# Performance work log

Measured on AMD Instinct MI355X. Metric: run time of the kernel, lower is better.

Reference implementation:

```python
import jax, jax.numpy as jnp
import numpy as np

N_HEADS = 16


def setup_inputs() -> dict:
    key = jax.random.key(0)
    ks = jax.random.split(key, 5)
    B, S, D = 2, 2048, 1024
    scale = 1.0 / np.sqrt(D)
    return {
        "x": jax.random.normal(ks[0], (B, S, D), dtype=jnp.float32),
        "w_in": jax.random.normal(ks[1], (3 * D, D), dtype=jnp.float32) * scale,
        "b_in": jax.random.normal(ks[2], (3 * D,), dtype=jnp.float32) * 0.01,
        "w_out": jax.random.normal(ks[3], (D, D), dtype=jnp.float32) * scale,
        "b_out": jax.random.normal(ks[4], (D,), dtype=jnp.float32) * 0.01,
        "mask": 1,
    }


def reference(x, w_in, b_in, w_out, b_out, mask):
    b, s, d = x.shape
    h = N_HEADS
    dh = d // h
    # fused QKV projection (torch Linear: x @ W^T + b)
    qkv = jnp.einsum("bsd,ed->bse", x, w_in) + b_in  # [b, s, 3d]
    q, k, v = jnp.split(qkv, 3, axis=-1)
    # [b, s, d] -> [b, h, s, dh]
    q = q.reshape(b, s, h, dh).transpose(0, 2, 1, 3)
    k = k.reshape(b, s, h, dh).transpose(0, 2, 1, 3)
    v = v.reshape(b, s, h, dh).transpose(0, 2, 1, 3)
    att = jnp.einsum("bhqd,bhkd->bhqk", q, k)
    if mask:
        causal = jnp.triu(jnp.ones((s, s), dtype=bool), k=1)
        att = jnp.where(causal, -jnp.inf, att)
    att = att / jnp.sqrt(jnp.asarray(dh, att.dtype))
    att = jax.nn.softmax(att, axis=-1)
    out = jnp.einsum("bhqk,bhkd->bhqd", att, v)  # [b, h, s, dh]
    out = out.transpose(0, 2, 1, 3).reshape(b, s, d)
    return jnp.einsum("bsd,ed->bse", out, w_out) + b_out
```

## Files before the change

kernel.cpp:

```cpp
#include <hip/hip_runtime.h>
#include <hip/hip_bf16.h>
#include <cmath>

typedef __hip_bfloat16 bf16;
typedef short v8s __attribute__((ext_vector_type(8)));
typedef short v4s __attribute__((ext_vector_type(4)));
typedef float v4f __attribute__((ext_vector_type(4)));
typedef float v16f __attribute__((ext_vector_type(16)));
typedef unsigned v4u __attribute__((ext_vector_type(4)));

#define AS1(p) ((__attribute__((address_space(1))) void*)(p))
#define AS3(p) ((__attribute__((address_space(3))) void*)(p))

__device__ __forceinline__ v4f mfma_bf16(v8s a, v8s b, v4f c) {
    return __builtin_amdgcn_mfma_f32_16x16x32_bf16(a, b, c, 0, 0, 0);
}
__device__ __forceinline__ v16f mfma32(v8s a, v8s b, v16f c) {
    return __builtin_amdgcn_mfma_f32_32x32x16_bf16(a, b, c, 0, 0, 0);
}

__device__ __forceinline__ short bf16_bits(float f) {
    return __builtin_bit_cast(short, __float2bfloat16(f));
}

__device__ __forceinline__ v8s pack4(unsigned a, unsigned b, unsigned c, unsigned d) {
    v4u u = {a, b, c, d};
    return __builtin_bit_cast(v8s, u);
}

__global__ __launch_bounds__(256)
void cvt_all(const float* __restrict__ x, const float* __restrict__ w_in,
             const float* __restrict__ w_out, bf16* __restrict__ xb,
             bf16* __restrict__ wib, bf16* __restrict__ wob)
{
    const int i = blockIdx.x * 256 + threadIdx.x;
    const float* src; bf16* dst; int j;
    if (i < 1048576)      { src = x;     dst = xb;  j = i; }
    else if (i < 1835008) { src = w_in;  dst = wib; j = i - 1048576; }
    else                  { src = w_out; dst = wob; j = i - 1835008; }
    const float4 v = ((const float4*)src)[j];
    v4s p;
    p.x = bf16_bits(v.x); p.y = bf16_bits(v.y);
    p.z = bf16_bits(v.z); p.w = bf16_bits(v.w);
    ((v4s*)dst)[j] = p;
}

template<int NF>
__global__ __launch_bounds__(256)
void gemm_bt(const bf16* __restrict__ A, const bf16* __restrict__ Bt,
             const float* __restrict__ bias, bf16* __restrict__ C,
             float* __restrict__ Cf, int N, int K, int lda)
{
    constexpr int BN = NF * 32;
    __shared__ __align__(16) bf16 As[2][128 * 32];
    __shared__ __align__(16) bf16 Bs[2][BN * 32];

    const int t    = threadIdx.x;
    const int lane = t & 63;
    const int wave = t >> 6;
    const int l16  = lane & 15;
    const int quad = lane >> 4;
    const int m0   = blockIdx.y * 128;
    const int n0   = blockIdx.x * BN;
    const int wm   = (wave >> 1) * 64;
    const int wn   = (wave & 1) * (NF * 16);

    const v4f zf = {0.f, 0.f, 0.f, 0.f};
    v4f acc[4][NF];
#pragma unroll
    for (int i = 0; i < 4; ++i)
#pragma unroll
        for (int j = 0; j < NF; ++j) acc[i][j] = zf;

    const int sr = t >> 2;
    const int g  = ((t & 3) ^ ((sr >> 1) & 3)) * 8;
    const bf16* gA = A  + (size_t)(m0 + sr) * lda + g;
    const bf16* gB = Bt + (size_t)(n0 + sr) * K + g;

    auto stage = [&](int kt, int buf) {
        const int k0 = kt * 32;
        char* lA = (char*)&As[buf][0] + t * 16;
        char* lB = (char*)&Bs[buf][0] + t * 16;
        __builtin_amdgcn_global_load_lds(AS1(gA + k0),                    AS3(lA),        16, 0, 0);
        __builtin_amdgcn_global_load_lds(AS1(gA + (size_t)64 * lda + k0), AS3(lA + 4096), 16, 0, 0);
        __builtin_amdgcn_global_load_lds(AS1(gB + k0),                    AS3(lB),        16, 0, 0);
        if (NF == 4)
            __builtin_amdgcn_global_load_lds(AS1(gB + (size_t)64 * K + k0), AS3(lB + 4096), 16, 0, 0);
    };

    stage(0, 0);
    const int KT = K >> 5;
    const int xs = ((l16 >> 1) & 3) * 8;
    for (int kt = 0; kt < KT; ++kt) {
        const int buf = kt & 1;
        __syncthreads();
        if (kt + 1 < KT) stage(kt + 1, buf ^ 1);

        v8s af[4], bfr[NF];
#pragma unroll
        for (int mi = 0; mi < 4; ++mi)
            af[mi] = *(const v8s*)(&As[buf][0] + (wm + mi * 16 + l16) * 32
                                   + ((quad * 8) ^ xs));
#pragma unroll
        for (int ni = 0; ni < NF; ++ni)
            bfr[ni] = *(const v8s*)(&Bs[buf][0] + (wn + ni * 16 + l16) * 32
                                    + ((quad * 8) ^ xs));
#pragma unroll
        for (int mi = 0; mi < 4; ++mi)
#pragma unroll
            for (int ni = 0; ni < NF; ++ni)
                acc[mi][ni] = mfma_bf16(af[mi], bfr[ni], acc[mi][ni]);
    }

#pragma unroll
    for (int ni = 0; ni < NF; ++ni) {
        const int col = n0 + wn + ni * 16 + l16;
        const float bv = bias[col];
#pragma unroll
        for (int mi = 0; mi < 4; ++mi) {
#pragma unroll
            for (int r = 0; r < 4; ++r) {
                const int row = m0 + wm + mi * 16 + quad * 4 + r;
                const float fv = acc[mi][ni][r] + bv;
                if (Cf) Cf[(size_t)row * N + col] = fv;
                else    C [(size_t)row * N + col] = __float2bfloat16(fv);
            }
        }
    }
}

__global__ __launch_bounds__(256)
void vtrans(const bf16* __restrict__ qkv, bf16* __restrict__ Vt)
{
    __shared__ short Ts[64][72];
    const int t  = threadIdx.x;
    const int st = blockIdx.x;
    const int bh = blockIdx.y;
    const int b = bh >> 4, h = bh & 15;
    const int s0 = st * 64;
    {
        const int i = t >> 2, j0 = (t & 3) * 16;
        const bf16* src = qkv + (size_t)(b * 2048 + s0 + i) * 3072 + 2048 + h * 64 + j0;
        const v8s a0 = *(const v8s*)(src);
        const v8s a1 = *(const v8s*)(src + 8);
        *(v8s*)&Ts[i][j0]     = a0;
        *(v8s*)&Ts[i][j0 + 8] = a1;
    }
    __syncthreads();
    {
        const int d = t >> 2, seg = (t & 3) * 16;
        v8s o0, o1;
#pragma unroll
        for (int m = 0; m < 8; ++m) { o0[m] = Ts[seg + m][d]; o1[m] = Ts[seg + 8 + m][d]; }
        bf16* dst = Vt + (size_t)(bh * 64 + d) * 2048 + s0 + seg;
        *(v8s*)dst       = o0;
        *(v8s*)(dst + 8) = o1;
    }
}

#define M_STATIC 14.0f

__device__ __forceinline__ void softpack(v16f s, int kg0, int qg, bool mask, int hi,
                                         float& lsum, v8s& paE, v8s& paO)
{
    float p[16];
#pragma unroll
    for (int r = 0; r < 16; ++r) {
        float pv = __expf(fmaf(s[r], 0.125f, -M_STATIC));
        if (mask) {
            const int kg = kg0 + (r & 3) + 8 * (r >> 2) + 4 * hi;
            if (kg > qg) pv = 0.f;
        }
        lsum += pv;
        p[r] = pv;
    }
    unsigned P0[4], P1[4];
#pragma unroll
    for (int m = 0; m < 4; ++m) {
        asm("v_cvt_pk_bf16_f32 %0, %1, %2" : "=v"(P0[m]) : "v"(p[4 * m]),     "v"(p[4 * m + 1]));
        asm("v_cvt_pk_bf16_f32 %0, %1, %2" : "=v"(P1[m]) : "v"(p[4 * m + 2]), "v"(p[4 * m + 3]));
    }
    auto sA = __builtin_amdgcn_permlane32_swap(P0[0], P0[1], false, false);
    auto sB = __builtin_amdgcn_permlane32_swap(P1[0], P1[1], false, false);
    auto sC = __builtin_amdgcn_permlane32_swap(P0[2], P0[3], false, false);
    auto sD = __builtin_amdgcn_permlane32_swap(P1[2], P1[3], false, false);
    paE = pack4(sA[0], sB[0], sA[1], sB[1]);
    paO = pack4(sC[0], sD[0], sC[1], sD[1]);
}

__global__ __launch_bounds__(128)
void attn(bf16* __restrict__ qkv, const bf16* __restrict__ Vt)
{
    __shared__ __align__(16) bf16 Ks[2][64 * 64];
    __shared__ __align__(16) bf16 Vs[2][64 * 64];

    const int t    = threadIdx.x;
    const int lane = t & 63;
    const int w    = t >> 6;
    const int l31  = lane & 31;
    const int hi   = lane >> 5;
    const int id   = blockIdx.x;
    const int bh   = id & 31;
    const int qb   = 31 - (id >> 5);
    const int b = bh >> 4, h = bh & 15;
    const int T = qb + 1;
    const int rowq = qb * 64 + w * 32;
    const int qg   = rowq + l31;
    const int xr   = l31 & 7;

    v8s qf[4];
    {
        const bf16* Qb = qkv + (size_t)(b * 2048 + qg) * 3072 + h * 64 + hi * 8;
#pragma unroll
        for (int c = 0; c < 4; ++c) qf[c] = *(const v8s*)(Qb + c * 16);
    }

    const int sr  = t >> 3;
    const int swz = ((t & 7) ^ (sr & 7)) * 8;
    const bf16* kbase = qkv + (size_t)(b * 2048 + sr) * 3072 + 1024 + h * 64 + swz;
    const bf16* vbase = Vt + (size_t)(bh * 64 + sr) * 2048 + swz;

    auto stage = [&](int tile, int buf2) {
        char* kd = (char*)&Ks[buf2][0] + t * 16;
        char* vd = (char*)&Vs[buf2][0] + t * 16;
        const bf16* ks0 = kbase + (size_t)(tile * 64) * 3072;
        const bf16* vs0 = vbase + tile * 64;
#pragma unroll
        for (int i = 0; i < 4; ++i) {
            __builtin_amdgcn_global_load_lds(AS1(ks0 + (size_t)(16 * i) * 3072), AS3(kd + i * 2048), 16, 0, 0);
            __builtin_amdgcn_global_load_lds(AS1(vs0 + (size_t)(16 * i) * 2048), AS3(vd + i * 2048), 16, 0, 0);
        }
    };

    stage(0, 0);

    v16f o0 = {}, o1 = {};
    float lsum = 0.f;

    for (int tile = 0; tile < T; ++tile) {
        const int buf = tile & 1;
        __syncthreads();
        if (tile + 1 < T) stage(tile + 1, buf ^ 1);

        const bf16* Kb = &Ks[buf][0];
        const bf16* Vb = &Vs[buf][0];
        const bool last = (tile == T - 1);
        const bool do1  = (!last) || (w == 1);

        v16f s0 = {}, s1 = {};
#pragma unroll
        for (int c = 0; c < 4; ++c) {
            const v8s kf = *(const v8s*)(Kb + l31 * 64 + (((2 * c + hi) ^ xr) * 8));
            s0 = mfma32(kf, qf[c], s0);
        }
        if (do1) {
#pragma unroll
            for (int c = 0; c < 4; ++c) {
                const v8s kf = *(const v8s*)(Kb + (32 + l31) * 64 + (((2 * c + hi) ^ xr) * 8));
                s1 = mfma32(kf, qf[c], s1);
            }
        }

        v8s pa0, pa1, pa2, pa3;
        softpack(s0, tile * 64,      qg, last, hi, lsum, pa0, pa1);
        if (do1) softpack(s1, tile * 64 + 32, qg, last, hi, lsum, pa2, pa3);

        o0 = mfma32(pa0, *(const v8s*)(Vb + l31 * 64        + (((0 + hi) ^ xr) * 8)), o0);
        o1 = mfma32(pa0, *(const v8s*)(Vb + (32 + l31) * 64 + (((0 + hi) ^ xr) * 8)), o1);
        o0 = mfma32(pa1, *(const v8s*)(Vb + l31 * 64        + (((2 + hi) ^ xr) * 8)), o0);
        o1 = mfma32(pa1, *(const v8s*)(Vb + (32 + l31) * 64 + (((2 + hi) ^ xr) * 8)), o1);
        if (do1) {
            o0 = mfma32(pa2, *(const v8s*)(Vb + l31 * 64        + (((4 + hi) ^ xr) * 8)), o0);
            o1 = mfma32(pa2, *(const v8s*)(Vb + (32 + l31) * 64 + (((4 + hi) ^ xr) * 8)), o1);
            o0 = mfma32(pa3, *(const v8s*)(Vb + l31 * 64        + (((6 + hi) ^ xr) * 8)), o0);
            o1 = mfma32(pa3, *(const v8s*)(Vb + (32 + l31) * 64 + (((6 + hi) ^ xr) * 8)), o1);
        }
    }

    const float lt = lsum + __shfl_xor(lsum, 32);

    bf16* dst0 = qkv + (size_t)(b * 2048 + rowq) * 3072 + 2048 + h * 64 + l31;
#pragma unroll
    for (int r = 0; r < 16; ++r) {
        const int q = (r & 3) + 8 * (r >> 2) + 4 * hi;
        const float rs  = fmaxf(__shfl(lt, q), 1e-30f);
        const float inv = 1.0f / rs;
        bf16* dst = dst0 + (size_t)q * 3072;
        dst[0]  = __float2bfloat16(o0[r] * inv);
        dst[32] = __float2bfloat16(o1[r] * inv);
    }
}

extern "C" void kernel_launch(void* const* d_in, const int* in_sizes, int n_in,
                              void* d_out, int out_size, void* d_ws, size_t ws_size,
                              hipStream_t stream)
{
    (void)in_sizes; (void)n_in; (void)out_size; (void)ws_size;
    const float* x     = (const float*)d_in[0];
    const float* w_in  = (const float*)d_in[1];
    const float* b_in  = (const float*)d_in[2];
    const float* w_out = (const float*)d_in[3];
    const float* b_out = (const float*)d_in[4];
    float* out = (float*)d_out;

    bf16* ws     = (bf16*)d_ws;
    bf16* xb     = ws;
    bf16* w_inb  = xb     + (size_t)4096 * 1024;
    bf16* w_outb = w_inb  + (size_t)3072 * 1024;
    bf16* qkv    = w_outb + (size_t)1024 * 1024;
    bf16* vt     = (bf16*)d_out;

    cvt_all<<<8192, 256, 0, stream>>>(x, w_in, w_out, xb, w_inb, w_outb);

    gemm_bt<4><<<dim3(24, 32), dim3(256), 0, stream>>>(xb, w_inb, b_in, qkv, nullptr,
                                                       3072, 1024, 1024);
    vtrans<<<dim3(32, 32), dim3(256), 0, stream>>>(qkv, vt);
    attn<<<1024, 128, 0, stream>>>(qkv, vt);
    gemm_bt<2><<<dim3(16, 32), dim3(256), 0, stream>>>(qkv + 2048, w_outb, b_out, nullptr,
                                                       out, 1024, 1024, 3072);
}
```

Measured before the change: 197.8 us.

## Split attention key tiles across four waves with LDS reduction of partial outputs

The attention kernel moves from 2 to 4 waves per block. Each query half-tile is now handled by two waves that take alternating 32-key halves of each 64-key tile, and their partial O accumulators and row sums are combined through shared memory at the end. The K/V staging layout changes to a chunk-major arrangement with fewer loads per thread, and the explicit XOR swizzle on the fragment reads is dropped. This aims to raise parallelism and latency hiding per block, at the cost of an extra reduction pass, more LDS traffic, and possible bank conflicts in the new layout.

After: 196.9 us. Within noise of the previous version (-0.5%).

```diff
diff --git a/kernel.cpp b/kernel.cpp
--- a/kernel.cpp
+++ b/kernel.cpp
@@ -188,7 +188,7 @@
     paO = pack4(sC[0], sD[0], sC[1], sD[1]);
 }
 
-__global__ __launch_bounds__(128)
+__global__ __launch_bounds__(256, 4)
 void attn(bf16* __restrict__ qkv, const bf16* __restrict__ Vt)
 {
     __shared__ __align__(16) bf16 Ks[2][64 * 64];
@@ -197,6 +197,8 @@
     const int t    = threadIdx.x;
     const int lane = t & 63;
     const int w    = t >> 6;
+    const int wq   = w >> 1;
+    const int wk   = w & 1;
     const int l31  = lane & 31;
     const int hi   = lane >> 5;
     const int id   = blockIdx.x;
@@ -204,9 +206,9 @@
     const int qb   = 31 - (id >> 5);
     const int b = bh >> 4, h = bh & 15;
     const int T = qb + 1;
-    const int rowq = qb * 64 + w * 32;
-    const int qg   = rowq + l31;
-    const int xr   = l31 & 7;
+    const int rowq  = qb * 64 + wq * 32;
+    const int qg    = rowq + l31;
+    const int ndiag = 2 * qb + wq;
 
     v8s qf[4];
     {
@@ -215,79 +217,99 @@
         for (int c = 0; c < 4; ++c) qf[c] = *(const v8s*)(Qb + c * 16);
     }
 
-    const int sr  = t >> 3;
-    const int swz = ((t & 7) ^ (sr & 7)) * 8;
-    const bf16* kbase = qkv + (size_t)(b * 2048 + sr) * 3072 + 1024 + h * 64 + swz;
-    const bf16* vbase = Vt + (size_t)(bh * 64 + sr) * 2048 + swz;
-
-    auto stage = [&](int tile, int buf2) {
-        char* kd = (char*)&Ks[buf2][0] + t * 16;
-        char* vd = (char*)&Vs[buf2][0] + t * 16;
+    const int sl    = t & 31;
+    const int chunk = 2 * ((t >> 6) & 3) + ((t >> 5) & 1);
+    const bf16* kbase = qkv + (size_t)(b * 2048 + sl) * 3072 + 1024 + h * 64 + chunk * 8;
+    const bf16* vbase = Vt + (size_t)(bh * 64 + sl) * 2048 + chunk * 8;
+
+    auto stage = [&](int tile, int bufi) {
+        char* kd = (char*)&Ks[bufi][0] + t * 16;
+        char* vd = (char*)&Vs[bufi][0] + t * 16;
         const bf16* ks0 = kbase + (size_t)(tile * 64) * 3072;
         const bf16* vs0 = vbase + tile * 64;
-#pragma unroll
-        for (int i = 0; i < 4; ++i) {
-            __builtin_amdgcn_global_load_lds(AS1(ks0 + (size_t)(16 * i) * 3072), AS3(kd + i * 2048), 16, 0, 0);
-            __builtin_amdgcn_global_load_lds(AS1(vs0 + (size_t)(16 * i) * 2048), AS3(vd + i * 2048), 16, 0, 0);
-        }
+        __builtin_amdgcn_global_load_lds(AS1(ks0),                   AS3(kd),        16, 0, 0);
+        __builtin_amdgcn_global_load_lds(AS1(ks0 + (size_t)32*3072), AS3(kd + 4096), 16, 0, 0);
+        __builtin_amdgcn_global_load_lds(AS1(vs0),                   AS3(vd),        16, 0, 0);
+        __builtin_amdgcn_global_load_lds(AS1(vs0 + (size_t)32*2048), AS3(vd + 4096), 16, 0, 0);
     };
 
     stage(0, 0);
 
     v16f o0 = {}, o1 = {};
     float lsum = 0.f;
+    const int kfoff = wk * 2048 + lane * 8;
+    const int vb0   = wk * 1024 + lane * 8;
 
     for (int tile = 0; tile < T; ++tile) {
         const int buf = tile & 1;
         __syncthreads();
         if (tile + 1 < T) stage(tile + 1, buf ^ 1);
 
-        const bf16* Kb = &Ks[buf][0];
-        const bf16* Vb = &Vs[buf][0];
-        const bool last = (tile == T - 1);
-        const bool do1  = (!last) || (w == 1);
-
-        v16f s0 = {}, s1 = {};
-#pragma unroll
-        for (int c = 0; c < 4; ++c) {
-            const v8s kf = *(const v8s*)(Kb + l31 * 64 + (((2 * c + hi) ^ xr) * 8));
-            s0 = mfma32(kf, qf[c], s0);
-        }
-        if (do1) {
-#pragma unroll
-            for (int c = 0; c < 4; ++c) {
-                const v8s kf = *(const v8s*)(Kb + (32 + l31) * 64 + (((2 * c + hi) ^ xr) * 8));
-                s1 = mfma32(kf, qf[c], s1);
-            }
-        }
-
-        v8s pa0, pa1, pa2, pa3;
-        softpack(s0, tile * 64,      qg, last, hi, lsum, pa0, pa1);
-        if (do1) softpack(s1, tile * 64 + 32, qg, last, hi, lsum, pa2, pa3);
-
-        o0 = mfma32(pa0, *(const v8s*)(Vb + l31 * 64        + (((0 + hi) ^ xr) * 8)), o0);
-        o1 = mfma32(pa0, *(const v8s*)(Vb + (32 + l31) * 64 + (((0 + hi) ^ xr) * 8)), o1);
-        o0 = mfma32(pa1, *(const v8s*)(Vb + l31 * 64        + (((2 + hi) ^ xr) * 8)), o0);
-        o1 = mfma32(pa1, *(const v8s*)(Vb + (32 + l31) * 64 + (((2 + hi) ^ xr) * 8)), o1);
-        if (do1) {
-            o0 = mfma32(pa2, *(const v8s*)(Vb + l31 * 64        + (((4 + hi) ^ xr) * 8)), o0);
-            o1 = mfma32(pa2, *(const v8s*)(Vb + (32 + l31) * 64 + (((4 + hi) ^ xr) * 8)), o1);
-            o0 = mfma32(pa3, *(const v8s*)(Vb + l31 * 64        + (((6 + hi) ^ xr) * 8)), o0);
-            o1 = mfma32(pa3, *(const v8s*)(Vb + (32 + l31) * 64 + (((6 + hi) ^ xr) * 8)), o1);
-        }
-    }
-
-    const float lt = lsum + __shfl_xor(lsum, 32);
-
-    bf16* dst0 = qkv + (size_t)(b * 2048 + rowq) * 3072 + 2048 + h * 64 + l31;
-#pragma unroll
-    for (int r = 0; r < 16; ++r) {
-        const int q = (r & 3) + 8 * (r >> 2) + 4 * hi;
-        const float rs  = fmaxf(__shfl(lt, q), 1e-30f);
-        const float inv = 1.0f / rs;
-        bf16* dst = dst0 + (size_t)q * 3072;
-        dst[0]  = __float2bfloat16(o0[r] * inv);
-        dst[32] = __float2bfloat16(o1[r] * inv);
+        const int m_ = 2 * tile + wk;
+        if (m_ <= ndiag) {
+            const bf16* Kb = &Ks[buf][0];
+            const bf16* Vb = &Vs[buf][0];
+
+            v16f s = {};
+#pragma unroll
+            for (int c = 0; c < 4; ++c)
+                s = mfma32(*(const v8s*)(Kb + kfoff + c * 512), qf[c], s);
+
+            v8s paE, paO;
+            softpack(s, tile * 64 + 32 * wk, qg, m_ == ndiag, hi, lsum, paE, paO);
+
+            o0 = mfma32(paE, *(const v8s*)(Vb + vb0),            o0);
+            o1 = mfma32(paE, *(const v8s*)(Vb + vb0 + 4 * 512),  o1);
+            o0 = mfma32(paO, *(const v8s*)(Vb + vb0 + 512),      o0);
+            o1 = mfma32(paO, *(const v8s*)(Vb + vb0 + 5 * 512),  o1);
+        }
+    }
+
+    __syncthreads();
+    float* Rp = (float*)&Ks[0][0];
+    float* Lp = (float*)&Vs[0][0];
+    if (wk) {
+        float* R = Rp + wq * 2048 + lane * 32;
+#pragma unroll
+        for (int j = 0; j < 4; ++j) {
+            v4f a = { o0[4*j], o0[4*j+1], o0[4*j+2], o0[4*j+3] };
+            ((v4f*)R)[j ^ (lane & 7)] = a;
+        }
+#pragma unroll
+        for (int j = 0; j < 4; ++j) {
+            v4f a = { o1[4*j], o1[4*j+1], o1[4*j+2], o1[4*j+3] };
+            ((v4f*)R)[(4 + j) ^ (lane & 7)] = a;
+        }
+        Lp[wq * 64 + lane] = lsum;
+    }
+    __syncthreads();
+    if (!wk) {
+        const float* R = Rp + wq * 2048 + lane * 32;
+#pragma unroll
+        for (int j = 0; j < 4; ++j) {
+            v4f a = ((const v4f*)R)[j ^ (lane & 7)];
+#pragma unroll
+            for (int e = 0; e < 4; ++e) o0[4*j + e] += a[e];
+        }
+#pragma unroll
+        for (int j = 0; j < 4; ++j) {
+            v4f a = ((const v4f*)R)[(4 + j) ^ (lane & 7)];
+#pragma unroll
+            for (int e = 0; e < 4; ++e) o1[4*j + e] += a[e];
+        }
+        lsum += Lp[wq * 64 + lane];
+        const float lt = lsum + __shfl_xor(lsum, 32);
+
+        bf16* dst0 = qkv + (size_t)(b * 2048 + rowq) * 3072 + 2048 + h * 64 + l31;
+#pragma unroll
+        for (int r = 0; r < 16; ++r) {
+            const int q = (r & 3) + 8 * (r >> 2) + 4 * hi;
+            const float rs  = fmaxf(__shfl(lt, q), 1e-30f);
+            const float inv = 1.0f / rs;
+            bf16* dst = dst0 + (size_t)q * 3072;
+            dst[0]  = __float2bfloat16(o0[r] * inv);
+            dst[32] = __float2bfloat16(o1[r] * inv);
+        }
     }
 }
 
@@ -315,7 +337,7 @@
     gemm_bt<4><<<dim3(24, 32), dim3(256), 0, stream>>>(xb, w_inb, b_in, qkv, nullptr,
                                                        3072, 1024, 1024);
     vtrans<<<dim3(32, 32), dim3(256), 0, stream>>>(qkv, vt);
-    attn<<<1024, 128, 0, stream>>>(qkv, vt);
+    attn<<<1024, 256, 0, stream>>>(qkv, vt);
     gemm_bt<2><<<dim3(16, 32), dim3(256), 0, stream>>>(qkv + 2048, w_outb, b_out, nullptr,
                                                        out, 1024, 1024, 3072);
 }
```
